# Kernel optimization log

Hardware: AMD Instinct MI355X
Metric: run time of the kernel (lower is better)

Reference implementation:

```python
import jax, jax.numpy as jnp
import numpy as np

IN_F = 1024
HID = 1024
OUT_F = 1024


def setup_inputs() -> dict:
    key = jax.random.key(0)
    ks = jax.random.split(key, 6)
    B, S = 64, 512
    x = jax.random.normal(ks[0], (B, S, IN_F), dtype=jnp.float32)
    hidden_first = jnp.zeros((B, HID), dtype=jnp.float32)
    lim1 = 1.0 / np.sqrt(IN_F + HID)
    lim2 = 1.0 / np.sqrt(HID)
    W_ih = jax.random.uniform(ks[1], (HID, IN_F + HID), minval=-lim1, maxval=lim1, dtype=jnp.float32)
    b_ih = jax.random.uniform(ks[2], (HID,), minval=-lim1, maxval=lim1, dtype=jnp.float32)
    W_ho = jax.random.uniform(ks[3], (OUT_F, HID), minval=-lim2, maxval=lim2, dtype=jnp.float32)
    b_ho = jax.random.uniform(ks[4], (OUT_F,), minval=-lim2, maxval=lim2, dtype=jnp.float32)
    return {"x": x, "hidden_first": hidden_first, "W_ih": W_ih, "b_ih": b_ih, "W_ho": W_ho, "b_ho": b_ho}


def reference(x, hidden_first, W_ih, b_ih, W_ho, b_ho):
    # x: [B, S, F] -> time-major [S, B, F]
    xt = jnp.swapaxes(x, 0, 1)
    # Split in2hidden weight into input and hidden blocks to avoid per-step concat
    W_x = W_ih[:, :IN_F]   # [H, F]
    W_h = W_ih[:, IN_F:]   # [H, H]
    # Precompute input projections for all timesteps in one big GEMM
    x_proj = jnp.einsum('sbf,hf->sbh', xt, W_x) + b_ih  # [S, B, H]

    def step(h, xp):
        h_new = jnp.tanh(xp + h @ W_h.T)
        out_t = h_new @ W_ho.T + b_ho
        return h_new, out_t

    _, outs = jax.lax.scan(step, hidden_first, x_proj)  # outs: [S, B, O]
    return jnp.swapaxes(outs, 0, 1)  # [B, S, O]
```

## Files before the change

### kernel.cpp

```cpp
#include <hip/hip_runtime.h>
#include <stdint.h>

typedef __attribute__((ext_vector_type(8))) short short8_t;
typedef __attribute__((ext_vector_type(4))) float f32x4_t;
typedef __attribute__((ext_vector_type(4))) unsigned int u32x4_t;

__device__ __forceinline__ unsigned short f2bf_u(float f) {
  unsigned int u = __float_as_uint(f);
  unsigned int r = (u + 0x7fff + ((u >> 16) & 1)) >> 16;
  return (unsigned short)r;
}
__device__ __forceinline__ float bf2f(unsigned short s) {
  return __uint_as_float(((unsigned int)s) << 16);
}
__device__ __forceinline__ short8_t pack8(float4 a, float4 b) {
  short8_t r;
  r[0]=(short)f2bf_u(a.x); r[1]=(short)f2bf_u(a.y); r[2]=(short)f2bf_u(a.z); r[3]=(short)f2bf_u(a.w);
  r[4]=(short)f2bf_u(b.x); r[5]=(short)f2bf_u(b.y); r[6]=(short)f2bf_u(b.z); r[7]=(short)f2bf_u(b.w);
  return r;
}
__device__ __forceinline__ void gl_lds16(const void* g, void* l) {
  __builtin_amdgcn_global_load_lds(
      (const __attribute__((address_space(1))) unsigned int*)g,
      (__attribute__((address_space(3))) unsigned int*)l, 16, 0, 0);
}

__global__ void k_prep_x(const float* __restrict__ src, unsigned short* __restrict__ dst) {
  int i = blockIdx.x * blockDim.x + threadIdx.x;
  if (i >= 4194304) return;
  const float4* s = (const float4*)src + (size_t)i * 2;
  float4 a = s[0], b = s[1];
  *(short8_t*)(dst + (size_t)i * 8) = pack8(a, b);
}

__global__ void k_prep_w(const float* __restrict__ Wih, const float* __restrict__ Who,
                         unsigned short* __restrict__ Wxbf, unsigned short* __restrict__ Whobf,
                         u32x4_t* __restrict__ hx2) {
  int tid = blockIdx.x * blockDim.x + threadIdx.x;
  if (tid < 131072) {
    int n = tid >> 7, c = tid & 127;
    const float* s = Wih + (size_t)n * 2048 + c * 8;
    float4 a = *(const float4*)s, b = *(const float4*)(s + 4);
    *(short8_t*)(Wxbf + (size_t)n * 1024 + c * 8) = pack8(a, b);
  } else {
    int j = tid - 131072;
    int n = j >> 7, c = j & 127;
    const float* s = Who + (size_t)n * 1024 + c * 8;
    float4 a = *(const float4*)s, b = *(const float4*)(s + 4);
    *(short8_t*)(Whobf + (size_t)n * 1024 + c * 8) = pack8(a, b);
  }
  if (tid < 32768) {
    u32x4_t z; z[0] = 0; z[1] = 0; z[2] = 0; z[3] = 0;
    hx2[tid] = z;
  }
}

template <bool OUT_BF16>
__global__ __launch_bounds__(256, 2) void k_gemm_bt(
    const unsigned short* __restrict__ A, const unsigned short* __restrict__ Bw,
    const float* __restrict__ bias, void* __restrict__ Cout) {
  constexpr int K = 1024, N = 1024;
  __shared__ unsigned short sm[8192];
  const int tid = threadIdx.x;
  const int wave = tid >> 6, lane = tid & 63;
  const int tm = blockIdx.y * 128, tn = blockIdx.x * 128;
  const int wm = wave >> 1, wn = wave & 1;

  f32x4_t acc[4][4];
#pragma unroll
  for (int i = 0; i < 4; i++)
#pragma unroll
    for (int j = 0; j < 4; j++) acc[i][j] = (f32x4_t){0.f, 0.f, 0.f, 0.f};

  char* ldsA = (char*)sm;
  char* ldsB = (char*)sm + 8192;
  const int cc = ((lane & 3) ^ ((lane >> 3) & 3)) * 8;
  const int rs = lane >> 2;

  for (int k0 = 0; k0 < K; k0 += 32) {
    __syncthreads();
#pragma unroll
    for (int c = 0; c < 2; c++) {
      int r0 = c * 64 + wave * 16;
      int r = r0 + rs;
      gl_lds16(A + (size_t)(tm + r) * K + (k0 + cc), ldsA + r0 * 64);
      gl_lds16(Bw + (size_t)(tn + r) * K + (k0 + cc), ldsB + r0 * 64);
    }
    __builtin_amdgcn_s_waitcnt(0);
    __syncthreads();

    short8_t af[4], bf[4];
#pragma unroll
    for (int mt = 0; mt < 4; mt++) {
      int r = wm * 64 + mt * 16 + (lane & 15);
      int slot = (((lane >> 4) ^ (((lane & 15) >> 1) & 3))) * 16;
      af[mt] = *(const short8_t*)(ldsA + r * 64 + slot);
    }
#pragma unroll
    for (int nt = 0; nt < 4; nt++) {
      int r = wn * 64 + nt * 16 + (lane & 15);
      int slot = (((lane >> 4) ^ (((lane & 15) >> 1) & 3))) * 16;
      bf[nt] = *(const short8_t*)(ldsB + r * 64 + slot);
    }
#pragma unroll
    for (int mt = 0; mt < 4; mt++)
#pragma unroll
      for (int nt = 0; nt < 4; nt++)
        acc[mt][nt] = __builtin_amdgcn_mfma_f32_16x16x32_bf16(af[mt], bf[nt], acc[mt][nt], 0, 0, 0);
  }

#pragma unroll
  for (int nt = 0; nt < 4; nt++) {
    int n = tn + wn * 64 + nt * 16 + (lane & 15);
    float bs = bias[n];
#pragma unroll
    for (int mt = 0; mt < 4; mt++) {
      int rowb = tm + wm * 64 + mt * 16 + ((lane >> 4) << 2);
      f32x4_t v = acc[mt][nt];
#pragma unroll
      for (int q = 0; q < 4; q++) {
        float o = v[q] + bs;
        size_t off = (size_t)(rowb + q) * N + n;
        if (OUT_BF16) ((unsigned short*)Cout)[off] = f2bf_u(o);
        else          ((float*)Cout)[off] = o;
      }
    }
  }
}

__global__ __launch_bounds__(256, 1) void k_rnn(
    const float* __restrict__ Wih, const float* __restrict__ h0,
    const unsigned short* __restrict__ xproj, unsigned short* __restrict__ Hall,
    char* __restrict__ hx2) {
  const int bid = blockIdx.x;
  const int g = (bid & 7) >> 1;
  const int rank = ((bid >> 3) << 1) | (bid & 1);
  const int tid = threadIdx.x;
  const int wave = tid >> 6, lane = tid & 63;
  const int nw = rank * 64 + wave * 16;
  const int b0 = g * 16;

  __shared__ unsigned short hs[16][1032];
  __shared__ unsigned short hsOut[16][68];

  short8_t bfrag[32];
  {
    const int n = nw + (lane & 15);
    const float* wrow = Wih + (size_t)n * 2048 + 1024 + ((lane >> 4) * 8);
#pragma unroll
    for (int kt = 0; kt < 32; kt++) {
      float4 f0 = *(const float4*)(wrow + kt * 32);
      float4 f1 = *(const float4*)(wrow + kt * 32 + 4);
      bfrag[kt] = pack8(f0, f1);
    }
  }

  const int row = tid >> 4, c16 = tid & 15;
  const char* hxb = hx2 + g * 65536;
  const unsigned voffc = (unsigned)(row * 256 + c16 * 16);

  for (int t = 0; t < 512; t++) {
    unsigned short xr[4];
#pragma unroll
    for (int q = 0; q < 4; q++) {
      int b = b0 + ((lane >> 4) << 2) + q;
      xr[q] = xproj[((size_t)b * 512 + t) * 1024 + nw + (lane & 15)];
    }

    if (t > 0) {
      *(unsigned long long*)&hs[row][(rank * 16 + c16) * 4] =
          *(const unsigned long long*)&hsOut[row][c16 * 4];
      const unsigned tg = (unsigned)t;
      const unsigned so = ((t - 1) & 1) ? 262144u : 0u;
      unsigned done = 1u << rank;
      u32x4_t r[16];
#pragma unroll
      for (int j = 0; j < 16; j++) { r[j][0] = 0; r[j][1] = 0; r[j][2] = 0; r[j][3] = 0; }
      while (done != 0xFFFFu) {
#pragma unroll
        for (int j = 0; j < 16; j++) {
          if (!((done >> j) & 1)) {
            asm volatile("global_load_dwordx4 %0, %1, %2 sc0 sc1"
                         : "=v"(r[j])
                         : "v"(so + (unsigned)(j << 12) + voffc), "s"(hxb)
                         : "memory");
          }
        }
        asm volatile("s_waitcnt vmcnt(0)"
                     : "+v"(r[0]), "+v"(r[1]), "+v"(r[2]), "+v"(r[3]),
                       "+v"(r[4]), "+v"(r[5]), "+v"(r[6]), "+v"(r[7]),
                       "+v"(r[8]), "+v"(r[9]), "+v"(r[10]), "+v"(r[11]),
                       "+v"(r[12]), "+v"(r[13]), "+v"(r[14]), "+v"(r[15]));
#pragma unroll
        for (int j = 0; j < 16; j++) {
          if (!((done >> j) & 1) && r[j][1] == tg && r[j][3] == tg) {
            *(unsigned long long*)&hs[row][(j * 16 + c16) * 4] =
                (unsigned long long)r[j][0] | ((unsigned long long)r[j][2] << 32);
            done |= 1u << j;
          }
        }
      }
    } else {
      const float* s = h0 + (size_t)(b0 + row) * 1024 + c16 * 8;
#pragma unroll
      for (int j = 0; j < 8; j++) {
        float4 a = *(const float4*)(s + j * 128);
        float4 b = *(const float4*)(s + j * 128 + 4);
        *(short8_t*)&hs[row][c16 * 8 + j * 128] = pack8(a, b);
      }
    }
    __syncthreads();

    f32x4_t acc0 = {0.f, 0.f, 0.f, 0.f}, acc1 = {0.f, 0.f, 0.f, 0.f};
    {
      const char* abase = (const char*)&hs[lane & 15][0] + ((lane >> 4) * 16);
#pragma unroll
      for (int kt = 0; kt < 32; kt += 2) {
        short8_t a0 = *(const short8_t*)(abase + kt * 64);
        acc0 = __builtin_amdgcn_mfma_f32_16x16x32_bf16(a0, bfrag[kt], acc0, 0, 0, 0);
        short8_t a1 = *(const short8_t*)(abase + (kt + 1) * 64);
        acc1 = __builtin_amdgcn_mfma_f32_16x16x32_bf16(a1, bfrag[kt + 1], acc1, 0, 0, 0);
      }
    }

#pragma unroll
    for (int q = 0; q < 4; q++) {
      int bl = ((lane >> 4) << 2) + q;
      float p = acc0[q] + acc1[q] + bf2f(xr[q]);
      float e = __expf(2.0f * p);
      float th = 1.0f - 2.0f / (e + 1.0f);
      hsOut[bl][wave * 16 + (lane & 15)] = f2bf_u(th);
    }
    __syncthreads();

    {
      unsigned long long vv = *(const unsigned long long*)&hsOut[row][c16 * 4];
      size_t hall_off = ((size_t)(b0 + row) * 512 + t) * 1024 + rank * 64 + c16 * 4;
      *(unsigned long long*)(Hall + hall_off) = vv;
      u32x4_t line;
      line[0] = (unsigned)vv;         line[1] = (unsigned)(t + 1);
      line[2] = (unsigned)(vv >> 32); line[3] = (unsigned)(t + 1);
      const unsigned sow = (t & 1) ? 262144u : 0u;
      asm volatile("global_store_dwordx4 %0, %1, %2 sc0 sc1"
                   :: "v"(sow + (unsigned)(rank << 12) + voffc), "v"(line), "s"(hxb)
                   : "memory");
    }
  }
}

extern "C" void kernel_launch(void* const* d_in, const int* in_sizes, int n_in,
                              void* d_out, int out_size, void* d_ws, size_t ws_size,
                              hipStream_t stream) {
  const float* x   = (const float*)d_in[0];
  const float* h0  = (const float*)d_in[1];
  const float* Wih = (const float*)d_in[2];
  const float* bih = (const float*)d_in[3];
  const float* Who = (const float*)d_in[4];
  const float* bho = (const float*)d_in[5];

  char* ws = (char*)d_ws;
  unsigned short* Xbf   = (unsigned short*)ws;
  unsigned short* Hall  = (unsigned short*)ws;
  unsigned short* xproj = (unsigned short*)(ws + 67108864);
  unsigned short* Wxbf  = (unsigned short*)(ws + 134217728);
  unsigned short* Whobf = (unsigned short*)(ws + 136314880);
  char*           hx2   = ws + 138412032;

  k_prep_x<<<16384, 256, 0, stream>>>(x, Xbf);
  k_prep_w<<<1024, 256, 0, stream>>>(Wih, Who, Wxbf, Whobf, (u32x4_t*)hx2);
  k_gemm_bt<true ><<<dim3(8, 256), 256, 0, stream>>>(Xbf, Wxbf, bih, (void*)xproj);
  k_rnn<<<64, 256, 0, stream>>>(Wih, h0, xproj, Hall, hx2);
  k_gemm_bt<false><<<dim3(8, 256), 256, 0, stream>>>(Hall, Whobf, bho, d_out);
}
```

Measured before the change: 1.955 ms.

## Regroup RNN blocks into 8x8 groups with XCD-aware cache-coherence exchange

Reorganises the recurrent kernel from 4 groups of 16 blocks (16 batch rows, 64 hidden columns each) into 8 groups of 8 blocks (8 batch rows, 128 hidden columns each). This halves the number of peers each block polls per step. At startup each block reads its XCD id from a hardware register and publishes it to a table, so it knows which peers share its XCD. Peers on the same XCD are polled with sc0-only loads, which can hit the shared L2, and only peers on other XCDs use sc0 sc1 system-coherent loads. Producers store both ways, and pollers fall back to coherent loads after 32 rounds. The cost is a startup handshake, a doubled store, half-wasted MFMA rows (only 8 of 16 batch rows are used), and reliance on XCD placement and coherence behaviour that must hold for correctness.

Result: slower. 2.309 ms (+18.1%).

```diff
diff --git a/kernel.cpp b/kernel.cpp
--- a/kernel.cpp
+++ b/kernel.cpp
@@ -35,7 +35,7 @@
 
 __global__ void k_prep_w(const float* __restrict__ Wih, const float* __restrict__ Who,
                          unsigned short* __restrict__ Wxbf, unsigned short* __restrict__ Whobf,
-                         u32x4_t* __restrict__ hx2) {
+                         u32x4_t* __restrict__ hx) {
   int tid = blockIdx.x * blockDim.x + threadIdx.x;
   if (tid < 131072) {
     int n = tid >> 7, c = tid & 127;
@@ -49,9 +49,9 @@
     float4 a = *(const float4*)s, b = *(const float4*)(s + 4);
     *(short8_t*)(Whobf + (size_t)n * 1024 + c * 8) = pack8(a, b);
   }
-  if (tid < 32768) {
+  if (tid < 32784) {
     u32x4_t z; z[0] = 0; z[1] = 0; z[2] = 0; z[3] = 0;
-    hx2[tid] = z;
+    hx[tid] = z;
   }
 }
 
@@ -131,82 +131,113 @@
 __global__ __launch_bounds__(256, 1) void k_rnn(
     const float* __restrict__ Wih, const float* __restrict__ h0,
     const unsigned short* __restrict__ xproj, unsigned short* __restrict__ Hall,
-    char* __restrict__ hx2) {
+    char* __restrict__ hx) {
   const int bid = blockIdx.x;
-  const int g = (bid & 7) >> 1;
-  const int rank = ((bid >> 3) << 1) | (bid & 1);
+  const int g = bid & 7;
+  const int rank = bid >> 3;
   const int tid = threadIdx.x;
   const int wave = tid >> 6, lane = tid & 63;
-  const int nw = rank * 64 + wave * 16;
-  const int b0 = g * 16;
+  const int b0 = g * 8;
+  const int nw = rank * 128 + wave * 32;
 
   __shared__ unsigned short hs[16][1032];
-  __shared__ unsigned short hsOut[16][68];
-
-  short8_t bfrag[32];
+  __shared__ unsigned short hsOut[8][132];
+  __shared__ int slowLds;
+
   {
-    const int n = nw + (lane & 15);
+    int xcd = __builtin_amdgcn_s_getreg(6164);
+    int myval = 256 + (xcd & 15);
+    int* table = (int*)(hx + 524288);
+    if (tid == 0) {
+      __hip_atomic_store(&table[bid], myval, __ATOMIC_RELAXED, __HIP_MEMORY_SCOPE_AGENT);
+      int sm = 0;
+      for (int j = 0; j < 8; j++) {
+        if (j == rank) continue;
+        int v;
+        do {
+          v = __hip_atomic_load(&table[j * 8 + g], __ATOMIC_RELAXED, __HIP_MEMORY_SCOPE_AGENT);
+        } while (v < 256);
+        if (v != myval) sm |= 1 << j;
+      }
+      slowLds = sm;
+    }
+  }
+
+  short8_t bfrag[2][32];
+#pragma unroll
+  for (int ct = 0; ct < 2; ct++) {
+    const int n = nw + ct * 16 + (lane & 15);
     const float* wrow = Wih + (size_t)n * 2048 + 1024 + ((lane >> 4) * 8);
 #pragma unroll
     for (int kt = 0; kt < 32; kt++) {
       float4 f0 = *(const float4*)(wrow + kt * 32);
       float4 f1 = *(const float4*)(wrow + kt * 32 + 4);
-      bfrag[kt] = pack8(f0, f1);
-    }
-  }
-
-  const int row = tid >> 4, c16 = tid & 15;
-  const char* hxb = hx2 + g * 65536;
-  const unsigned voffc = (unsigned)(row * 256 + c16 * 16);
+      bfrag[ct][kt] = pack8(f0, f1);
+    }
+  }
+
+  for (int i = tid; i < 4128; i += 256) ((int*)&hs[8][0])[i] = 0;
+  __syncthreads();
+  const int slowInit = slowLds;
+
+  const int row = tid >> 5, c32 = tid & 31;
+  const char* hxg = hx + g * 32768;
+  const unsigned voffc = (unsigned)(tid * 16);
 
   for (int t = 0; t < 512; t++) {
-    unsigned short xr[4];
-#pragma unroll
-    for (int q = 0; q < 4; q++) {
-      int b = b0 + ((lane >> 4) << 2) + q;
-      xr[q] = xproj[((size_t)b * 512 + t) * 1024 + nw + (lane & 15)];
-    }
+    unsigned short xr[2][4];
+#pragma unroll
+    for (int ct = 0; ct < 2; ct++)
+#pragma unroll
+      for (int q = 0; q < 4; q++) {
+        int bl = (((lane >> 4) << 2) + q) & 7;
+        xr[ct][q] = xproj[((size_t)(b0 + bl) * 512 + t) * 1024 + nw + ct * 16 + (lane & 15)];
+      }
 
     if (t > 0) {
-      *(unsigned long long*)&hs[row][(rank * 16 + c16) * 4] =
-          *(const unsigned long long*)&hsOut[row][c16 * 4];
+      *(unsigned long long*)&hs[row][rank * 128 + c32 * 4] =
+          *(const unsigned long long*)&hsOut[row][c32 * 4];
       const unsigned tg = (unsigned)t;
-      const unsigned so = ((t - 1) & 1) ? 262144u : 0u;
-      unsigned done = 1u << rank;
-      u32x4_t r[16];
-#pragma unroll
-      for (int j = 0; j < 16; j++) { r[j][0] = 0; r[j][1] = 0; r[j][2] = 0; r[j][3] = 0; }
-      while (done != 0xFFFFu) {
-#pragma unroll
-        for (int j = 0; j < 16; j++) {
-          if (!((done >> j) & 1)) {
-            asm volatile("global_load_dwordx4 %0, %1, %2 sc0 sc1"
-                         : "=v"(r[j])
-                         : "v"(so + (unsigned)(j << 12) + voffc), "s"(hxb)
-                         : "memory");
+      const unsigned sb = ((t - 1) & 1) ? 262144u : 0u;
+      unsigned pend = 0xFFu & ~(1u << rank);
+      int slow = slowInit;
+      int rounds = 0;
+      u32x4_t rf[8];
+#pragma unroll
+      for (int j = 0; j < 8; j++) { rf[j][0] = 0; rf[j][1] = 0; rf[j][2] = 0; rf[j][3] = 0; }
+      while (pend) {
+#pragma unroll
+        for (int j = 0; j < 8; j++) {
+          if ((pend >> j) & 1) {
+            unsigned off = sb + (unsigned)(j * 4096) + voffc;
+            if ((slow >> j) & 1)
+              asm volatile("global_load_dwordx4 %0, %1, %2 sc0 sc1"
+                           : "=v"(rf[j]) : "v"(off), "s"(hxg) : "memory");
+            else
+              asm volatile("global_load_dwordx4 %0, %1, %2 sc0"
+                           : "=v"(rf[j]) : "v"(off), "s"(hxg) : "memory");
           }
         }
         asm volatile("s_waitcnt vmcnt(0)"
-                     : "+v"(r[0]), "+v"(r[1]), "+v"(r[2]), "+v"(r[3]),
-                       "+v"(r[4]), "+v"(r[5]), "+v"(r[6]), "+v"(r[7]),
-                       "+v"(r[8]), "+v"(r[9]), "+v"(r[10]), "+v"(r[11]),
-                       "+v"(r[12]), "+v"(r[13]), "+v"(r[14]), "+v"(r[15]));
-#pragma unroll
-        for (int j = 0; j < 16; j++) {
-          if (!((done >> j) & 1) && r[j][1] == tg && r[j][3] == tg) {
-            *(unsigned long long*)&hs[row][(j * 16 + c16) * 4] =
-                (unsigned long long)r[j][0] | ((unsigned long long)r[j][2] << 32);
-            done |= 1u << j;
+                     : "+v"(rf[0]), "+v"(rf[1]), "+v"(rf[2]), "+v"(rf[3]),
+                       "+v"(rf[4]), "+v"(rf[5]), "+v"(rf[6]), "+v"(rf[7]));
+#pragma unroll
+        for (int j = 0; j < 8; j++) {
+          if (((pend >> j) & 1) && rf[j][1] == tg && rf[j][3] == tg) {
+            *(unsigned long long*)&hs[row][j * 128 + c32 * 4] =
+                (unsigned long long)rf[j][0] | ((unsigned long long)rf[j][2] << 32);
+            pend &= ~(1u << j);
           }
         }
+        if (++rounds == 32) slow = 0xFF;
       }
     } else {
-      const float* s = h0 + (size_t)(b0 + row) * 1024 + c16 * 8;
+      const float* s = h0 + (size_t)(b0 + row) * 1024 + c32 * 4;
 #pragma unroll
       for (int j = 0; j < 8; j++) {
         float4 a = *(const float4*)(s + j * 128);
-        float4 b = *(const float4*)(s + j * 128 + 4);
-        *(short8_t*)&hs[row][c16 * 8 + j * 128] = pack8(a, b);
+        unsigned short* d = &hs[row][j * 128 + c32 * 4];
+        d[0] = f2bf_u(a.x); d[1] = f2bf_u(a.y); d[2] = f2bf_u(a.z); d[3] = f2bf_u(a.w);
       }
     }
     __syncthreads();
@@ -215,35 +246,39 @@
     {
       const char* abase = (const char*)&hs[lane & 15][0] + ((lane >> 4) * 16);
 #pragma unroll
-      for (int kt = 0; kt < 32; kt += 2) {
-        short8_t a0 = *(const short8_t*)(abase + kt * 64);
-        acc0 = __builtin_amdgcn_mfma_f32_16x16x32_bf16(a0, bfrag[kt], acc0, 0, 0, 0);
-        short8_t a1 = *(const short8_t*)(abase + (kt + 1) * 64);
-        acc1 = __builtin_amdgcn_mfma_f32_16x16x32_bf16(a1, bfrag[kt + 1], acc1, 0, 0, 0);
+      for (int kt = 0; kt < 32; kt++) {
+        short8_t a = *(const short8_t*)(abase + kt * 64);
+        acc0 = __builtin_amdgcn_mfma_f32_16x16x32_bf16(a, bfrag[0][kt], acc0, 0, 0, 0);
+        acc1 = __builtin_amdgcn_mfma_f32_16x16x32_bf16(a, bfrag[1][kt], acc1, 0, 0, 0);
       }
     }
 
 #pragma unroll
     for (int q = 0; q < 4; q++) {
       int bl = ((lane >> 4) << 2) + q;
-      float p = acc0[q] + acc1[q] + bf2f(xr[q]);
-      float e = __expf(2.0f * p);
-      float th = 1.0f - 2.0f / (e + 1.0f);
-      hsOut[bl][wave * 16 + (lane & 15)] = f2bf_u(th);
+      if (bl < 8) {
+        float p0 = acc0[q] + bf2f(xr[0][q]);
+        float e0 = __expf(2.0f * p0);
+        hsOut[bl][wave * 32 + (lane & 15)] = f2bf_u(1.0f - 2.0f / (e0 + 1.0f));
+        float p1 = acc1[q] + bf2f(xr[1][q]);
+        float e1 = __expf(2.0f * p1);
+        hsOut[bl][wave * 32 + 16 + (lane & 15)] = f2bf_u(1.0f - 2.0f / (e1 + 1.0f));
+      }
     }
     __syncthreads();
 
     {
-      unsigned long long vv = *(const unsigned long long*)&hsOut[row][c16 * 4];
-      size_t hall_off = ((size_t)(b0 + row) * 512 + t) * 1024 + rank * 64 + c16 * 4;
-      *(unsigned long long*)(Hall + hall_off) = vv;
+      unsigned long long vv = *(const unsigned long long*)&hsOut[row][c32 * 4];
       u32x4_t line;
       line[0] = (unsigned)vv;         line[1] = (unsigned)(t + 1);
       line[2] = (unsigned)(vv >> 32); line[3] = (unsigned)(t + 1);
-      const unsigned sow = (t & 1) ? 262144u : 0u;
+      unsigned off = ((t & 1) ? 262144u : 0u) + (unsigned)(rank * 4096) + voffc;
+      asm volatile("global_store_dwordx4 %0, %1, %2 sc0"
+                   :: "v"(off), "v"(line), "s"(hxg) : "memory");
       asm volatile("global_store_dwordx4 %0, %1, %2 sc0 sc1"
-                   :: "v"(sow + (unsigned)(rank << 12) + voffc), "v"(line), "s"(hxb)
-                   : "memory");
+                   :: "v"(off), "v"(line), "s"(hxg) : "memory");
+      size_t hall_off = ((size_t)(b0 + row) * 512 + t) * 1024 + rank * 128 + c32 * 4;
+      *(unsigned long long*)(Hall + hall_off) = vv;
     }
   }
 }
@@ -264,11 +299,11 @@
   unsigned short* xproj = (unsigned short*)(ws + 67108864);
   unsigned short* Wxbf  = (unsigned short*)(ws + 134217728);
   unsigned short* Whobf = (unsigned short*)(ws + 136314880);
-  char*           hx2   = ws + 138412032;
+  char*           hx    = ws + 138412032;
 
   k_prep_x<<<16384, 256, 0, stream>>>(x, Xbf);
-  k_prep_w<<<1024, 256, 0, stream>>>(Wih, Who, Wxbf, Whobf, (u32x4_t*)hx2);
+  k_prep_w<<<1024, 256, 0, stream>>>(Wih, Who, Wxbf, Whobf, (u32x4_t*)hx);
   k_gemm_bt<true ><<<dim3(8, 256), 256, 0, stream>>>(Xbf, Wxbf, bih, (void*)xproj);
-  k_rnn<<<64, 256, 0, stream>>>(Wih, h0, xproj, Hall, hx2);
+  k_rnn<<<64, 256, 0, stream>>>(Wih, h0, xproj, Hall, hx);
   k_gemm_bt<false><<<dim3(8, 256), 256, 0, stream>>>(Hall, Whobf, bho, d_out);
 }
```
